# Performance work log

Hardware: AMD Instinct MI355X
Metric: run time of the kernel (lower is better)

## Reference

```python
import jax, jax.numpy as jnp
import numpy as np

NUM_STAGES = 3
EPS = 1e-6


def _l2norm(x, axis):
    return x / (EPS + jnp.linalg.norm(x, axis=axis, keepdims=True))


def _l1norm(x, axis):
    return x / (EPS + jnp.sum(x, axis=axis, keepdims=True))


def setup_inputs() -> dict:
    key = jax.random.key(0)
    k1, k2 = jax.random.split(key)
    B, C, H, W, K = 16, 512, 64, 64, 64
    feats = jax.random.normal(k1, (B, C, H, W), dtype=jnp.float32)
    # bases buffer: N(0, sqrt(2/K)) then l2-normalized along channel dim (done in reference)
    bases = jax.random.normal(k2, (1, C, K), dtype=jnp.float32) * np.sqrt(2.0 / K)
    return {"feats": feats, "bases": bases}


def reference(feats, bases):
    B, C, H, W = feats.shape
    f = feats.reshape(B, C, H * W)              # [B, C, N]
    b = _l2norm(bases, axis=1)                  # match buffer init normalization
    b = jnp.broadcast_to(b, (B, C, b.shape[2])) # [B, C, K]
    attention = None
    for _ in range(NUM_STAGES):
        attention = jnp.einsum('bcn,bck->bnk', f, b)        # [B, N, K]
        attention = jax.nn.softmax(attention, axis=2)
        attention_normed = _l1norm(attention, axis=1)
        b = jnp.einsum('bcn,bnk->bck', f, attention_normed)  # [B, C, K]
        b = _l2norm(b, axis=1)
    # EM loop runs under torch.no_grad in the original
    b = jax.lax.stop_gradient(b)
    attention = jax.lax.stop_gradient(attention)
    feats_recon = jnp.einsum('bck,bnk->bcn', b, attention)   # [B, C, N]
    return feats_recon.reshape(B, C, H, W)
```

## Files before the change

kernel.cpp:

```cpp
#include <hip/hip_runtime.h>
#include <stdint.h>

#define B_ 16
#define C_ 512
#define N_ 4096
#define K_ 64
#define NUM_STAGES 3

typedef __bf16 bf16x8 __attribute__((ext_vector_type(8)));
typedef float f32x4 __attribute__((ext_vector_type(4)));

__device__ __forceinline__ uint16_t f2bf(float x) {
  union { float f; uint32_t u; } v; v.f = x;
  uint32_t r = (v.u + 0x7FFFu + ((v.u >> 16) & 1u)) >> 16;
  return (uint16_t)r;
}

__device__ __forceinline__ void async16(const uint16_t* g, uint16_t* l) {
  __builtin_amdgcn_global_load_lds(
      (const __attribute__((address_space(1))) unsigned int*)g,
      (__attribute__((address_space(3))) unsigned int*)l, 16, 0, 0);
}

__global__ __launch_bounds__(256) void k_prep(const float* __restrict__ feats,
                                              uint16_t* __restrict__ f16,
                                              uint16_t* __restrict__ fT16) {
  __shared__ uint16_t tile[64][65];
  int b = blockIdx.z, c0 = blockIdx.y * 64, n0 = blockIdx.x * 64;
  int t = threadIdx.x;
  const float* src = feats + ((size_t)b * C_ + c0) * N_ + n0;
  uint16_t* dst = f16 + ((size_t)b * C_ + c0) * N_ + n0;
  int cl = t >> 4;
  int nl = (t & 15) * 4;
#pragma unroll
  for (int i = 0; i < 4; ++i) {
    int c = cl + 16 * i;
    float4 v = *(const float4*)(src + (size_t)c * N_ + nl);
    ushort4 x;
    x.x = f2bf(v.x); x.y = f2bf(v.y); x.z = f2bf(v.z); x.w = f2bf(v.w);
    *(ushort4*)(dst + (size_t)c * N_ + nl) = x;
    tile[c][nl + 0] = x.x; tile[c][nl + 1] = x.y;
    tile[c][nl + 2] = x.z; tile[c][nl + 3] = x.w;
  }
  __syncthreads();
  uint16_t* dstT = fT16 + ((size_t)b * N_ + n0) * C_ + c0;
#pragma unroll
  for (int i = 0; i < 4; ++i) {
    int n = cl + 16 * i;
    int c = nl;
    ushort4 y;
    y.x = tile[c + 0][n]; y.y = tile[c + 1][n];
    y.z = tile[c + 2][n]; y.w = tile[c + 3][n];
    *(ushort4*)(dstT + (size_t)n * C_ + c) = y;
  }
}

__global__ __launch_bounds__(256) void k_init_basis(const float* __restrict__ bases,
                                                    uint16_t* __restrict__ basis,
                                                    uint16_t* __restrict__ basisT) {
  int b = blockIdx.x;
  int t = threadIdx.x;
  __shared__ float red[256];
  __shared__ float inv[64];
  int k = t & 63;
  float s = 0.f;
  for (int c = (t >> 6); c < C_; c += 4) {
    float v = bases[c * K_ + k];
    s += v * v;
  }
  red[t] = s;
  __syncthreads();
  if (t < 64) {
    float tot = red[t] + red[t + 64] + red[t + 128] + red[t + 192];
    inv[t] = 1.f / (1e-6f + sqrtf(tot));
  }
  __syncthreads();
  uint16_t* ob = basis + (size_t)b * C_ * K_;
  for (int i = 0; i < (C_ * K_) / 256; ++i) {
    int idx = t + 256 * i;
    int kk = idx & 63;
    ob[idx] = f2bf(bases[idx] * inv[kk]);
  }
  uint16_t* obT = basisT + (size_t)b * K_ * C_;
  for (int i = 0; i < (C_ * K_) / 256; ++i) {
    int idx = t + 256 * i;
    int kk = idx >> 9;
    int cc = idx & 511;
    obT[idx] = f2bf(bases[cc * K_ + kk] * inv[kk]);
  }
}

__global__ __launch_bounds__(256) void k_gemm1(const uint16_t* __restrict__ fT,
                                               const uint16_t* __restrict__ basisT,
                                               uint16_t* __restrict__ attn,
                                               uint16_t* __restrict__ attnT) {
  __shared__ __attribute__((aligned(16))) uint16_t ldsA[64 * 64];
  __shared__ __attribute__((aligned(16))) uint16_t ldsB[64 * 64];
  int b = blockIdx.y;
  int n0 = blockIdx.x * 64;
  int t = threadIdx.x;
  int w = t >> 6, lane = t & 63, l15 = lane & 15, quad = lane >> 4;
  const uint16_t* A = fT + ((size_t)b * N_ + n0) * C_;
  const uint16_t* Bm = basisT + (size_t)b * K_ * C_;
  f32x4 acc[4] = {};
  for (int cs = 0; cs < C_; cs += 64) {
    __syncthreads();
#pragma unroll
    for (int r = 0; r < 2; ++r) {
      int e = r * 256 + t;
      int row = e >> 3, ch = e & 7;
      int sch = (ch + row) & 7;
      async16(A + (size_t)row * C_ + cs + sch * 8, ldsA + (r * 256 + (t & 192)) * 8);
    }
#pragma unroll
    for (int r = 0; r < 2; ++r) {
      int e = r * 256 + t;
      int row = e >> 3, ch = e & 7;
      int sch = (ch + row) & 7;
      async16(Bm + (size_t)row * C_ + cs + sch * 8, ldsB + (r * 256 + (t & 192)) * 8);
    }
    __syncthreads();
#pragma unroll
    for (int s = 0; s < 2; ++s) {
      int cc = s * 4 + quad;
      int ra = 16 * w + l15;
      bf16x8 af = *(const bf16x8*)(ldsA + ra * 64 + ((cc - ra) & 7) * 8);
#pragma unroll
      for (int t4 = 0; t4 < 4; ++t4) {
        int rb = 16 * t4 + l15;
        bf16x8 bv = *(const bf16x8*)(ldsB + rb * 64 + ((cc - rb) & 7) * 8);
        acc[t4] = __builtin_amdgcn_mfma_f32_16x16x32_bf16(af, bv, acc[t4], 0, 0, 0);
      }
    }
  }
  float p[4][4];
#pragma unroll
  for (int r = 0; r < 4; ++r) {
    float m = fmaxf(fmaxf(acc[0][r], acc[1][r]), fmaxf(acc[2][r], acc[3][r]));
    m = fmaxf(m, __shfl_xor(m, 1));
    m = fmaxf(m, __shfl_xor(m, 2));
    m = fmaxf(m, __shfl_xor(m, 4));
    m = fmaxf(m, __shfl_xor(m, 8));
    float s = 0.f;
#pragma unroll
    for (int t4 = 0; t4 < 4; ++t4) { p[t4][r] = __expf(acc[t4][r] - m); s += p[t4][r]; }
    s += __shfl_xor(s, 1); s += __shfl_xor(s, 2);
    s += __shfl_xor(s, 4); s += __shfl_xor(s, 8);
    float inv = 1.f / s;
#pragma unroll
    for (int t4 = 0; t4 < 4; ++t4) p[t4][r] *= inv;
  }
  uint16_t* oa = attn + ((size_t)b * N_ + n0 + 16 * w + quad * 4) * K_;
#pragma unroll
  for (int r = 0; r < 4; ++r) {
#pragma unroll
    for (int t4 = 0; t4 < 4; ++t4) oa[(size_t)r * K_ + 16 * t4 + l15] = f2bf(p[t4][r]);
  }
#pragma unroll
  for (int t4 = 0; t4 < 4; ++t4) {
    ushort4 y;
    y.x = f2bf(p[t4][0]); y.y = f2bf(p[t4][1]);
    y.z = f2bf(p[t4][2]); y.w = f2bf(p[t4][3]);
    *(ushort4*)(attnT + ((size_t)b * K_ + 16 * t4 + l15) * N_ + n0 + 16 * w + quad * 4) = y;
  }
}

__global__ __launch_bounds__(256) void k_gemm2(const uint16_t* __restrict__ f16,
                                               const uint16_t* __restrict__ attnT,
                                               float* __restrict__ brawT) {
  __shared__ __attribute__((aligned(16))) uint16_t ldsA[32 * 64];
  __shared__ __attribute__((aligned(16))) uint16_t ldsB[64 * 64];
  int b = blockIdx.z;
  int c0 = blockIdx.x * 32;
  int slice = blockIdx.y;
  int ns0 = slice * 1024;
  int t = threadIdx.x, w = t >> 6, lane = t & 63, l15 = lane & 15, quad = lane >> 4;
  int h = w >> 1, kh = w & 1;
  const uint16_t* A = f16 + ((size_t)b * C_ + c0) * N_;
  const uint16_t* Bm = attnT + (size_t)b * K_ * N_;
  f32x4 acc[2] = {};
  for (int ns = ns0; ns < ns0 + 1024; ns += 64) {
    __syncthreads();
    {
      int row = t >> 3, ch = t & 7;
      int sch = (ch + row) & 7;
      async16(A + (size_t)row * N_ + ns + sch * 8, ldsA + (t & 192) * 8);
    }
#pragma unroll
    for (int r = 0; r < 2; ++r) {
      int e = r * 256 + t;
      int row = e >> 3, ch = e & 7;
      int sch = (ch + row) & 7;
      async16(Bm + (size_t)row * N_ + ns + sch * 8, ldsB + (r * 256 + (t & 192)) * 8);
    }
    __syncthreads();
#pragma unroll
    for (int s = 0; s < 2; ++s) {
      int cc = s * 4 + quad;
      int ra = 16 * h + l15;
      bf16x8 af = *(const bf16x8*)(ldsA + ra * 64 + ((cc - ra) & 7) * 8);
#pragma unroll
      for (int t2 = 0; t2 < 2; ++t2) {
        int rb = 32 * kh + 16 * t2 + l15;
        bf16x8 bv = *(const bf16x8*)(ldsB + rb * 64 + ((cc - rb) & 7) * 8);
        acc[t2] = __builtin_amdgcn_mfma_f32_16x16x32_bf16(af, bv, acc[t2], 0, 0, 0);
      }
    }
  }
  float* out = brawT + ((size_t)slice * B_ + b) * K_ * C_;
#pragma unroll
  for (int t2 = 0; t2 < 2; ++t2) {
    int k = 32 * kh + 16 * t2 + l15;
    float4 v = make_float4(acc[t2][0], acc[t2][1], acc[t2][2], acc[t2][3]);
    *(float4*)(out + (size_t)k * C_ + c0 + 16 * h + quad * 4) = v;
  }
}

__global__ __launch_bounds__(256) void k_l2norm(const float* __restrict__ brawT,
                                                uint16_t* __restrict__ basisT) {
  int b = blockIdx.x;
  int t = threadIdx.x, w = t >> 6, lane = t & 63;
  for (int k = w; k < K_; k += 4) {
    float v[8];
#pragma unroll
    for (int j = 0; j < 8; ++j) v[j] = 0.f;
#pragma unroll
    for (int s = 0; s < 4; ++s) {
      const float* rs = brawT + (((size_t)s * B_ + b) * K_ + k) * C_ + lane * 8;
      float4 a = *(const float4*)(rs);
      float4 c4 = *(const float4*)(rs + 4);
      v[0] += a.x; v[1] += a.y; v[2] += a.z; v[3] += a.w;
      v[4] += c4.x; v[5] += c4.y; v[6] += c4.z; v[7] += c4.w;
    }
    float ss = 0.f;
#pragma unroll
    for (int j = 0; j < 8; ++j) ss += v[j] * v[j];
    ss += __shfl_xor(ss, 1); ss += __shfl_xor(ss, 2); ss += __shfl_xor(ss, 4);
    ss += __shfl_xor(ss, 8); ss += __shfl_xor(ss, 16); ss += __shfl_xor(ss, 32);
    float inv = 1.f / (1e-6f + sqrtf(ss));
    ushort4 y0, y1;
    y0.x = f2bf(v[0] * inv); y0.y = f2bf(v[1] * inv);
    y0.z = f2bf(v[2] * inv); y0.w = f2bf(v[3] * inv);
    y1.x = f2bf(v[4] * inv); y1.y = f2bf(v[5] * inv);
    y1.z = f2bf(v[6] * inv); y1.w = f2bf(v[7] * inv);
    uint16_t* o = basisT + ((size_t)b * K_ + k) * C_ + lane * 8;
    *(ushort4*)(o) = y0;
    *(ushort4*)(o + 4) = y1;
  }
}

__global__ __launch_bounds__(256) void k_transpose_basis(const uint16_t* __restrict__ basisT,
                                                         uint16_t* __restrict__ basis) {
  __shared__ uint16_t tile[64][65];
  int b = blockIdx.y, ct = blockIdx.x;
  int t = threadIdx.x;
  const uint16_t* src = basisT + (size_t)b * K_ * C_ + ct * 64;
  for (int i = 0; i < 16; ++i) {
    int idx = t + 256 * i;
    int k = idx >> 6, c = idx & 63;
    tile[k][c] = src[(size_t)k * C_ + c];
  }
  __syncthreads();
  uint16_t* dst = basis + (size_t)b * C_ * K_ + (size_t)ct * 64 * K_;
  for (int i = 0; i < 16; ++i) {
    int idx = t + 256 * i;
    int c = idx >> 6, k = idx & 63;
    dst[(size_t)c * K_ + k] = tile[k][c];
  }
}

__global__ __launch_bounds__(256) void k_recon(const uint16_t* __restrict__ attn,
                                               const uint16_t* __restrict__ basis,
                                               float* __restrict__ out) {
  __shared__ __attribute__((aligned(16))) uint16_t ldsA[64 * 64];
  __shared__ __attribute__((aligned(16))) uint16_t ldsB[64 * 64];
  int b = blockIdx.z, c0 = blockIdx.y * 64, n0 = blockIdx.x * 64;
  int t = threadIdx.x, w = t >> 6, lane = t & 63, l15 = lane & 15, quad = lane >> 4;
  const uint16_t* A = attn + ((size_t)b * N_ + n0) * K_;
  const uint16_t* Bm = basis + ((size_t)b * C_ + c0) * K_;
#pragma unroll
  for (int r = 0; r < 2; ++r) {
    int e = r * 256 + t;
    int row = e >> 3, ch = e & 7, sch = (ch + row) & 7;
    async16(A + (size_t)row * K_ + sch * 8, ldsA + (r * 256 + (t & 192)) * 8);
  }
#pragma unroll
  for (int r = 0; r < 2; ++r) {
    int e = r * 256 + t;
    int row = e >> 3, ch = e & 7, sch = (ch + row) & 7;
    async16(Bm + (size_t)row * K_ + sch * 8, ldsB + (r * 256 + (t & 192)) * 8);
  }
  f32x4 acc[4] = {};
  __syncthreads();
#pragma unroll
  for (int s = 0; s < 2; ++s) {
    int cc = s * 4 + quad;
    int ra = 16 * w + l15;
    bf16x8 af = *(const bf16x8*)(ldsA + ra * 64 + ((cc - ra) & 7) * 8);
#pragma unroll
    for (int t4 = 0; t4 < 4; ++t4) {
      int rb = 16 * t4 + l15;
      bf16x8 bv = *(const bf16x8*)(ldsB + rb * 64 + ((cc - rb) & 7) * 8);
      acc[t4] = __builtin_amdgcn_mfma_f32_16x16x32_bf16(af, bv, acc[t4], 0, 0, 0);
    }
  }
#pragma unroll
  for (int t4 = 0; t4 < 4; ++t4) {
    int c = c0 + 16 * t4 + l15;
    float4 v = make_float4(acc[t4][0], acc[t4][1], acc[t4][2], acc[t4][3]);
    *(float4*)(out + ((size_t)b * C_ + c) * N_ + n0 + 16 * w + quad * 4) = v;
  }
}

extern "C" void kernel_launch(void* const* d_in, const int* in_sizes, int n_in,
                              void* d_out, int out_size, void* d_ws, size_t ws_size,
                              hipStream_t stream) {
  const float* feats = (const float*)d_in[0];
  const float* bases = (const float*)d_in[1];
  float* out = (float*)d_out;
  char* ws = (char*)d_ws;
  uint16_t* f16 = (uint16_t*)(ws);
  uint16_t* fT16 = (uint16_t*)(ws + 67108864);
  uint16_t* attn = (uint16_t*)(ws + 134217728);
  uint16_t* attnT = (uint16_t*)(ws + 142606336);
  uint16_t* basis = (uint16_t*)(ws + 150994944);
  uint16_t* basisT = (uint16_t*)(ws + 152043520);
  float* brawT = (float*)(ws + 153092096);

  k_prep<<<dim3(64, 8, 16), 256, 0, stream>>>(feats, f16, fT16);
  k_init_basis<<<16, 256, 0, stream>>>(bases, basis, basisT);
  for (int st = 0; st < NUM_STAGES; ++st) {
    k_gemm1<<<dim3(64, 16), 256, 0, stream>>>(fT16, basisT, attn, attnT);
    k_gemm2<<<dim3(16, 4, 16), 256, 0, stream>>>(f16, attnT, brawT);
    k_l2norm<<<16, 256, 0, stream>>>(brawT, basisT);
    k_transpose_basis<<<dim3(8, 16), 256, 0, stream>>>(basisT, basis);
  }
  k_recon<<<dim3(64, 8, 16), 256, 0, stream>>>(attn, basis, out);
}
```

Measured before the change: 478.6 us.

## Enlarge GEMM tiles to 512 threads, skip redundant attn writes, batch prep tiles

gemm1 and recon now use 128-row N tiles with 512 threads, so each basis tile loaded into LDS serves twice as many rows. gemm2 is restructured to 128 channels by 64 K per block with 8 N-slices, so the f16 tile is reused across all K, and l2norm now sums 8 partial slices. gemm1 writes the row-major attention only on the last stage, dropping redundant stores in earlier stages. k_prep processes four 64-wide tiles per block with vectorized LDS writes. The trade-offs are fewer blocks per launch and gemm2 partial-sum stores that are now scalar and strided.

After: 507.4 us. 6.0% more time.

```diff
diff --git a/kernel.cpp b/kernel.cpp
--- a/kernel.cpp
+++ b/kernel.cpp
@@ -25,33 +25,36 @@
 __global__ __launch_bounds__(256) void k_prep(const float* __restrict__ feats,
                                               uint16_t* __restrict__ f16,
                                               uint16_t* __restrict__ fT16) {
-  __shared__ uint16_t tile[64][65];
-  int b = blockIdx.z, c0 = blockIdx.y * 64, n0 = blockIdx.x * 64;
-  int t = threadIdx.x;
-  const float* src = feats + ((size_t)b * C_ + c0) * N_ + n0;
-  uint16_t* dst = f16 + ((size_t)b * C_ + c0) * N_ + n0;
+  __shared__ uint16_t tile[64][68];
+  int b = blockIdx.z, c0 = blockIdx.y * 64, n0 = blockIdx.x * 256;
+  int t = threadIdx.x;
   int cl = t >> 4;
   int nl = (t & 15) * 4;
-#pragma unroll
-  for (int i = 0; i < 4; ++i) {
-    int c = cl + 16 * i;
-    float4 v = *(const float4*)(src + (size_t)c * N_ + nl);
-    ushort4 x;
-    x.x = f2bf(v.x); x.y = f2bf(v.y); x.z = f2bf(v.z); x.w = f2bf(v.w);
-    *(ushort4*)(dst + (size_t)c * N_ + nl) = x;
-    tile[c][nl + 0] = x.x; tile[c][nl + 1] = x.y;
-    tile[c][nl + 2] = x.z; tile[c][nl + 3] = x.w;
-  }
-  __syncthreads();
-  uint16_t* dstT = fT16 + ((size_t)b * N_ + n0) * C_ + c0;
-#pragma unroll
-  for (int i = 0; i < 4; ++i) {
-    int n = cl + 16 * i;
-    int c = nl;
-    ushort4 y;
-    y.x = tile[c + 0][n]; y.y = tile[c + 1][n];
-    y.z = tile[c + 2][n]; y.w = tile[c + 3][n];
-    *(ushort4*)(dstT + (size_t)n * C_ + c) = y;
+  for (int nt = 0; nt < 4; ++nt) {
+    int n0s = n0 + nt * 64;
+    const float* src = feats + ((size_t)b * C_ + c0) * N_ + n0s;
+    uint16_t* dst = f16 + ((size_t)b * C_ + c0) * N_ + n0s;
+    __syncthreads();
+#pragma unroll
+    for (int i = 0; i < 4; ++i) {
+      int c = cl + 16 * i;
+      float4 v = *(const float4*)(src + (size_t)c * N_ + nl);
+      ushort4 x;
+      x.x = f2bf(v.x); x.y = f2bf(v.y); x.z = f2bf(v.z); x.w = f2bf(v.w);
+      *(ushort4*)(dst + (size_t)c * N_ + nl) = x;
+      *(ushort4*)&tile[c][nl] = x;
+    }
+    __syncthreads();
+    uint16_t* dstT = fT16 + ((size_t)b * N_ + n0s) * C_ + c0;
+#pragma unroll
+    for (int i = 0; i < 4; ++i) {
+      int n = cl + 16 * i;
+      int c = nl;
+      ushort4 y;
+      y.x = tile[c + 0][n]; y.y = tile[c + 1][n];
+      y.z = tile[c + 2][n]; y.w = tile[c + 3][n];
+      *(ushort4*)(dstT + (size_t)n * C_ + c) = y;
+    }
   }
 }
 
@@ -90,14 +93,15 @@
   }
 }
 
-__global__ __launch_bounds__(256) void k_gemm1(const uint16_t* __restrict__ fT,
+__global__ __launch_bounds__(512) void k_gemm1(const uint16_t* __restrict__ fT,
                                                const uint16_t* __restrict__ basisT,
                                                uint16_t* __restrict__ attn,
-                                               uint16_t* __restrict__ attnT) {
-  __shared__ __attribute__((aligned(16))) uint16_t ldsA[64 * 64];
+                                               uint16_t* __restrict__ attnT,
+                                               int write_attn) {
+  __shared__ __attribute__((aligned(16))) uint16_t ldsA[128 * 64];
   __shared__ __attribute__((aligned(16))) uint16_t ldsB[64 * 64];
   int b = blockIdx.y;
-  int n0 = blockIdx.x * 64;
+  int n0 = blockIdx.x * 128;
   int t = threadIdx.x;
   int w = t >> 6, lane = t & 63, l15 = lane & 15, quad = lane >> 4;
   const uint16_t* A = fT + ((size_t)b * N_ + n0) * C_;
@@ -107,17 +111,15 @@
     __syncthreads();
 #pragma unroll
     for (int r = 0; r < 2; ++r) {
-      int e = r * 256 + t;
+      int e = r * 512 + t;
       int row = e >> 3, ch = e & 7;
       int sch = (ch + row) & 7;
-      async16(A + (size_t)row * C_ + cs + sch * 8, ldsA + (r * 256 + (t & 192)) * 8);
-    }
-#pragma unroll
-    for (int r = 0; r < 2; ++r) {
-      int e = r * 256 + t;
-      int row = e >> 3, ch = e & 7;
+      async16(A + (size_t)row * C_ + cs + sch * 8, ldsA + (r * 512 + (t & 448)) * 8);
+    }
+    {
+      int row = t >> 3, ch = t & 7;
       int sch = (ch + row) & 7;
-      async16(Bm + (size_t)row * C_ + cs + sch * 8, ldsB + (r * 256 + (t & 192)) * 8);
+      async16(Bm + (size_t)row * C_ + cs + sch * 8, ldsB + (t & 448) * 8);
     }
     __syncthreads();
 #pragma unroll
@@ -150,11 +152,13 @@
 #pragma unroll
     for (int t4 = 0; t4 < 4; ++t4) p[t4][r] *= inv;
   }
-  uint16_t* oa = attn + ((size_t)b * N_ + n0 + 16 * w + quad * 4) * K_;
-#pragma unroll
-  for (int r = 0; r < 4; ++r) {
-#pragma unroll
-    for (int t4 = 0; t4 < 4; ++t4) oa[(size_t)r * K_ + 16 * t4 + l15] = f2bf(p[t4][r]);
+  if (write_attn) {
+    uint16_t* oa = attn + ((size_t)b * N_ + n0 + 16 * w + quad * 4) * K_;
+#pragma unroll
+    for (int r = 0; r < 4; ++r) {
+#pragma unroll
+      for (int t4 = 0; t4 < 4; ++t4) oa[(size_t)r * K_ + 16 * t4 + l15] = f2bf(p[t4][r]);
+    }
   }
 #pragma unroll
   for (int t4 = 0; t4 < 4; ++t4) {
@@ -165,54 +169,55 @@
   }
 }
 
-__global__ __launch_bounds__(256) void k_gemm2(const uint16_t* __restrict__ f16,
+__global__ __launch_bounds__(512) void k_gemm2(const uint16_t* __restrict__ f16,
                                                const uint16_t* __restrict__ attnT,
                                                float* __restrict__ brawT) {
-  __shared__ __attribute__((aligned(16))) uint16_t ldsA[32 * 64];
-  __shared__ __attribute__((aligned(16))) uint16_t ldsB[64 * 64];
+  __shared__ __attribute__((aligned(16))) uint16_t ldsF[128 * 64];
+  __shared__ __attribute__((aligned(16))) uint16_t ldsP[64 * 64];
   int b = blockIdx.z;
-  int c0 = blockIdx.x * 32;
   int slice = blockIdx.y;
-  int ns0 = slice * 1024;
-  int t = threadIdx.x, w = t >> 6, lane = t & 63, l15 = lane & 15, quad = lane >> 4;
-  int h = w >> 1, kh = w & 1;
-  const uint16_t* A = f16 + ((size_t)b * C_ + c0) * N_;
-  const uint16_t* Bm = attnT + (size_t)b * K_ * N_;
-  f32x4 acc[2] = {};
-  for (int ns = ns0; ns < ns0 + 1024; ns += 64) {
-    __syncthreads();
+  int c0 = blockIdx.x * 128;
+  int t = threadIdx.x;
+  int w = t >> 6, lane = t & 63, l15 = lane & 15, quad = lane >> 4;
+  const uint16_t* F = f16 + ((size_t)b * C_ + c0) * N_;
+  const uint16_t* P = attnT + (size_t)b * K_ * N_;
+  f32x4 acc[4] = {};
+  int ns0 = slice * 512;
+  for (int ns = ns0; ns < ns0 + 512; ns += 64) {
+    __syncthreads();
+#pragma unroll
+    for (int r = 0; r < 2; ++r) {
+      int e = r * 512 + t;
+      int row = e >> 3, ch = e & 7;
+      int sch = (ch + row) & 7;
+      async16(F + (size_t)row * N_ + ns + sch * 8, ldsF + (r * 512 + (t & 448)) * 8);
+    }
     {
       int row = t >> 3, ch = t & 7;
       int sch = (ch + row) & 7;
-      async16(A + (size_t)row * N_ + ns + sch * 8, ldsA + (t & 192) * 8);
-    }
-#pragma unroll
-    for (int r = 0; r < 2; ++r) {
-      int e = r * 256 + t;
-      int row = e >> 3, ch = e & 7;
-      int sch = (ch + row) & 7;
-      async16(Bm + (size_t)row * N_ + ns + sch * 8, ldsB + (r * 256 + (t & 192)) * 8);
+      async16(P + (size_t)row * N_ + ns + sch * 8, ldsP + (t & 448) * 8);
     }
     __syncthreads();
 #pragma unroll
     for (int s = 0; s < 2; ++s) {
       int cc = s * 4 + quad;
-      int ra = 16 * h + l15;
-      bf16x8 af = *(const bf16x8*)(ldsA + ra * 64 + ((cc - ra) & 7) * 8);
-#pragma unroll
-      for (int t2 = 0; t2 < 2; ++t2) {
-        int rb = 32 * kh + 16 * t2 + l15;
-        bf16x8 bv = *(const bf16x8*)(ldsB + rb * 64 + ((cc - rb) & 7) * 8);
-        acc[t2] = __builtin_amdgcn_mfma_f32_16x16x32_bf16(af, bv, acc[t2], 0, 0, 0);
+      int rb = 16 * w + l15;
+      bf16x8 fv = *(const bf16x8*)(ldsF + rb * 64 + ((cc - rb) & 7) * 8);
+#pragma unroll
+      for (int kt = 0; kt < 4; ++kt) {
+        int ra = 16 * kt + l15;
+        bf16x8 av = *(const bf16x8*)(ldsP + ra * 64 + ((cc - ra) & 7) * 8);
+        acc[kt] = __builtin_amdgcn_mfma_f32_16x16x32_bf16(av, fv, acc[kt], 0, 0, 0);
       }
     }
   }
-  float* out = brawT + ((size_t)slice * B_ + b) * K_ * C_;
-#pragma unroll
-  for (int t2 = 0; t2 < 2; ++t2) {
-    int k = 32 * kh + 16 * t2 + l15;
-    float4 v = make_float4(acc[t2][0], acc[t2][1], acc[t2][2], acc[t2][3]);
-    *(float4*)(out + (size_t)k * C_ + c0 + 16 * h + quad * 4) = v;
+  float* outp = brawT + ((size_t)slice * B_ + b) * K_ * C_;
+#pragma unroll
+  for (int kt = 0; kt < 4; ++kt) {
+#pragma unroll
+    for (int r = 0; r < 4; ++r) {
+      outp[(size_t)(16 * kt + quad * 4 + r) * C_ + c0 + 16 * w + l15] = acc[kt][r];
+    }
   }
 }
 
@@ -225,7 +230,7 @@
 #pragma unroll
     for (int j = 0; j < 8; ++j) v[j] = 0.f;
 #pragma unroll
-    for (int s = 0; s < 4; ++s) {
+    for (int s = 0; s < 8; ++s) {
       const float* rs = brawT + (((size_t)s * B_ + b) * K_ + k) * C_ + lane * 8;
       float4 a = *(const float4*)(rs);
       float4 c4 = *(const float4*)(rs + 4);
@@ -269,26 +274,24 @@
   }
 }
 
-__global__ __launch_bounds__(256) void k_recon(const uint16_t* __restrict__ attn,
+__global__ __launch_bounds__(512) void k_recon(const uint16_t* __restrict__ attn,
                                                const uint16_t* __restrict__ basis,
                                                float* __restrict__ out) {
-  __shared__ __attribute__((aligned(16))) uint16_t ldsA[64 * 64];
+  __shared__ __attribute__((aligned(16))) uint16_t ldsA[128 * 64];
   __shared__ __attribute__((aligned(16))) uint16_t ldsB[64 * 64];
-  int b = blockIdx.z, c0 = blockIdx.y * 64, n0 = blockIdx.x * 64;
+  int b = blockIdx.z, c0 = blockIdx.y * 64, n0 = blockIdx.x * 128;
   int t = threadIdx.x, w = t >> 6, lane = t & 63, l15 = lane & 15, quad = lane >> 4;
   const uint16_t* A = attn + ((size_t)b * N_ + n0) * K_;
   const uint16_t* Bm = basis + ((size_t)b * C_ + c0) * K_;
 #pragma unroll
   for (int r = 0; r < 2; ++r) {
-    int e = r * 256 + t;
+    int e = r * 512 + t;
     int row = e >> 3, ch = e & 7, sch = (ch + row) & 7;
-    async16(A + (size_t)row * K_ + sch * 8, ldsA + (r * 256 + (t & 192)) * 8);
-  }
-#pragma unroll
-  for (int r = 0; r < 2; ++r) {
-    int e = r * 256 + t;
-    int row = e >> 3, ch = e & 7, sch = (ch + row) & 7;
-    async16(Bm + (size_t)row * K_ + sch * 8, ldsB + (r * 256 + (t & 192)) * 8);
+    async16(A + (size_t)row * K_ + sch * 8, ldsA + (r * 512 + (t & 448)) * 8);
+  }
+  {
+    int row = t >> 3, ch = t & 7, sch = (ch + row) & 7;
+    async16(Bm + (size_t)row * K_ + sch * 8, ldsB + (t & 448) * 8);
   }
   f32x4 acc[4] = {};
   __syncthreads();
@@ -327,13 +330,14 @@
   uint16_t* basisT = (uint16_t*)(ws + 152043520);
   float* brawT = (float*)(ws + 153092096);
 
-  k_prep<<<dim3(64, 8, 16), 256, 0, stream>>>(feats, f16, fT16);
+  k_prep<<<dim3(16, 8, 16), 256, 0, stream>>>(feats, f16, fT16);
   k_init_basis<<<16, 256, 0, stream>>>(bases, basis, basisT);
   for (int st = 0; st < NUM_STAGES; ++st) {
-    k_gemm1<<<dim3(64, 16), 256, 0, stream>>>(fT16, basisT, attn, attnT);
-    k_gemm2<<<dim3(16, 4, 16), 256, 0, stream>>>(f16, attnT, brawT);
+    k_gemm1<<<dim3(32, 16), 512, 0, stream>>>(fT16, basisT, attn, attnT,
+                                              st == NUM_STAGES - 1 ? 1 : 0);
+    k_gemm2<<<dim3(4, 8, 16), 512, 0, stream>>>(f16, attnT, brawT);
     k_l2norm<<<16, 256, 0, stream>>>(brawT, basisT);
     k_transpose_basis<<<dim3(8, 16), 256, 0, stream>>>(basisT, basis);
   }
-  k_recon<<<dim3(64, 8, 16), 256, 0, stream>>>(attn, basis, out);
-}
+  k_recon<<<dim3(32, 8, 16), 512, 0, stream>>>(attn, basis, out);
+}
```

## Fuse l2norm with basis transpose, skip unused attn writes, stage recon output

Applied to the files above, without the earlier changes.

Merges the l2norm and basis-transpose kernels into one kernel with a wider grid (16x16 blocks) that writes both basis layouts. The row-major attention is now written only in the last stage, since recon is its only consumer. The recon kernel stages its output tile in LDS so that global stores are coalesced rows. The LDS index expressions are rewritten in an equivalent form. In exchange, the fused kernel writes the row-major basis with strided scalar stores and adds an extra LDS round-trip in recon.

Result: faster. 448.4 us (-6.3%).

```diff
diff --git a/kernel.cpp b/kernel.cpp
--- a/kernel.cpp
+++ b/kernel.cpp
@@ -93,7 +93,8 @@
 __global__ __launch_bounds__(256) void k_gemm1(const uint16_t* __restrict__ fT,
                                                const uint16_t* __restrict__ basisT,
                                                uint16_t* __restrict__ attn,
-                                               uint16_t* __restrict__ attnT) {
+                                               uint16_t* __restrict__ attnT,
+                                               int write_attn) {
   __shared__ __attribute__((aligned(16))) uint16_t ldsA[64 * 64];
   __shared__ __attribute__((aligned(16))) uint16_t ldsB[64 * 64];
   int b = blockIdx.y;
@@ -124,11 +125,11 @@
     for (int s = 0; s < 2; ++s) {
       int cc = s * 4 + quad;
       int ra = 16 * w + l15;
-      bf16x8 af = *(const bf16x8*)(ldsA + ra * 64 + ((cc - ra) & 7) * 8);
+      bf16x8 af = *(const bf16x8*)(ldsA + (ra * 8 + ((cc - ra) & 7)) * 8);
 #pragma unroll
       for (int t4 = 0; t4 < 4; ++t4) {
         int rb = 16 * t4 + l15;
-        bf16x8 bv = *(const bf16x8*)(ldsB + rb * 64 + ((cc - rb) & 7) * 8);
+        bf16x8 bv = *(const bf16x8*)(ldsB + (rb * 8 + ((cc - rb) & 7)) * 8);
         acc[t4] = __builtin_amdgcn_mfma_f32_16x16x32_bf16(af, bv, acc[t4], 0, 0, 0);
       }
     }
@@ -150,11 +151,13 @@
 #pragma unroll
     for (int t4 = 0; t4 < 4; ++t4) p[t4][r] *= inv;
   }
-  uint16_t* oa = attn + ((size_t)b * N_ + n0 + 16 * w + quad * 4) * K_;
-#pragma unroll
-  for (int r = 0; r < 4; ++r) {
-#pragma unroll
-    for (int t4 = 0; t4 < 4; ++t4) oa[(size_t)r * K_ + 16 * t4 + l15] = f2bf(p[t4][r]);
+  if (write_attn) {
+    uint16_t* oa = attn + ((size_t)b * N_ + n0 + 16 * w + quad * 4) * K_;
+#pragma unroll
+    for (int r = 0; r < 4; ++r) {
+#pragma unroll
+      for (int t4 = 0; t4 < 4; ++t4) oa[(size_t)r * K_ + 16 * t4 + l15] = f2bf(p[t4][r]);
+    }
   }
 #pragma unroll
   for (int t4 = 0; t4 < 4; ++t4) {
@@ -198,11 +201,11 @@
     for (int s = 0; s < 2; ++s) {
       int cc = s * 4 + quad;
       int ra = 16 * h + l15;
-      bf16x8 af = *(const bf16x8*)(ldsA + ra * 64 + ((cc - ra) & 7) * 8);
+      bf16x8 af = *(const bf16x8*)(ldsA + (ra * 8 + ((cc - ra) & 7)) * 8);
 #pragma unroll
       for (int t2 = 0; t2 < 2; ++t2) {
         int rb = 32 * kh + 16 * t2 + l15;
-        bf16x8 bv = *(const bf16x8*)(ldsB + rb * 64 + ((cc - rb) & 7) * 8);
+        bf16x8 bv = *(const bf16x8*)(ldsB + (rb * 8 + ((cc - rb) & 7)) * 8);
         acc[t2] = __builtin_amdgcn_mfma_f32_16x16x32_bf16(af, bv, acc[t2], 0, 0, 0);
       }
     }
@@ -216,64 +219,64 @@
   }
 }
 
-__global__ __launch_bounds__(256) void k_l2norm(const float* __restrict__ brawT,
-                                                uint16_t* __restrict__ basisT) {
-  int b = blockIdx.x;
-  int t = threadIdx.x, w = t >> 6, lane = t & 63;
-  for (int k = w; k < K_; k += 4) {
-    float v[8];
-#pragma unroll
-    for (int j = 0; j < 8; ++j) v[j] = 0.f;
+__global__ __launch_bounds__(256) void k_l2fused(const float* __restrict__ brawT,
+                                                 uint16_t* __restrict__ basisT,
+                                                 uint16_t* __restrict__ basis) {
+  __shared__ float red[4][128];
+  __shared__ float invs[4];
+  int b = blockIdx.x, kg = blockIdx.y;
+  int t = threadIdx.x;
+  int c4 = (t & 127) * 4;
+  int khalf = t >> 7;
+  float4 bs[2];
+  float pr[2];
+#pragma unroll
+  for (int i = 0; i < 2; ++i) {
+    int k = kg * 4 + khalf * 2 + i;
+    float4 a = make_float4(0.f, 0.f, 0.f, 0.f);
 #pragma unroll
     for (int s = 0; s < 4; ++s) {
-      const float* rs = brawT + (((size_t)s * B_ + b) * K_ + k) * C_ + lane * 8;
-      float4 a = *(const float4*)(rs);
-      float4 c4 = *(const float4*)(rs + 4);
-      v[0] += a.x; v[1] += a.y; v[2] += a.z; v[3] += a.w;
-      v[4] += c4.x; v[5] += c4.y; v[6] += c4.z; v[7] += c4.w;
-    }
-    float ss = 0.f;
-#pragma unroll
-    for (int j = 0; j < 8; ++j) ss += v[j] * v[j];
-    ss += __shfl_xor(ss, 1); ss += __shfl_xor(ss, 2); ss += __shfl_xor(ss, 4);
-    ss += __shfl_xor(ss, 8); ss += __shfl_xor(ss, 16); ss += __shfl_xor(ss, 32);
-    float inv = 1.f / (1e-6f + sqrtf(ss));
-    ushort4 y0, y1;
-    y0.x = f2bf(v[0] * inv); y0.y = f2bf(v[1] * inv);
-    y0.z = f2bf(v[2] * inv); y0.w = f2bf(v[3] * inv);
-    y1.x = f2bf(v[4] * inv); y1.y = f2bf(v[5] * inv);
-    y1.z = f2bf(v[6] * inv); y1.w = f2bf(v[7] * inv);
-    uint16_t* o = basisT + ((size_t)b * K_ + k) * C_ + lane * 8;
-    *(ushort4*)(o) = y0;
-    *(ushort4*)(o + 4) = y1;
-  }
-}
-
-__global__ __launch_bounds__(256) void k_transpose_basis(const uint16_t* __restrict__ basisT,
-                                                         uint16_t* __restrict__ basis) {
-  __shared__ uint16_t tile[64][65];
-  int b = blockIdx.y, ct = blockIdx.x;
-  int t = threadIdx.x;
-  const uint16_t* src = basisT + (size_t)b * K_ * C_ + ct * 64;
-  for (int i = 0; i < 16; ++i) {
-    int idx = t + 256 * i;
-    int k = idx >> 6, c = idx & 63;
-    tile[k][c] = src[(size_t)k * C_ + c];
-  }
-  __syncthreads();
-  uint16_t* dst = basis + (size_t)b * C_ * K_ + (size_t)ct * 64 * K_;
-  for (int i = 0; i < 16; ++i) {
-    int idx = t + 256 * i;
-    int c = idx >> 6, k = idx & 63;
-    dst[(size_t)c * K_ + k] = tile[k][c];
+      const float* rp = brawT + (((size_t)s * B_ + b) * K_ + k) * C_ + c4;
+      float4 v = *(const float4*)rp;
+      a.x += v.x; a.y += v.y; a.z += v.z; a.w += v.w;
+    }
+    bs[i] = a;
+    pr[i] = a.x * a.x + a.y * a.y + a.z * a.z + a.w * a.w;
+  }
+  red[khalf * 2 + 0][t & 127] = pr[0];
+  red[khalf * 2 + 1][t & 127] = pr[1];
+  __syncthreads();
+  if (t < 4) {
+    float s = 0.f;
+#pragma unroll
+    for (int j = 0; j < 128; ++j) s += red[t][j];
+    invs[t] = 1.f / (1e-6f + sqrtf(s));
+  }
+  __syncthreads();
+#pragma unroll
+  for (int i = 0; i < 2; ++i) {
+    int kk = khalf * 2 + i;
+    int k = kg * 4 + kk;
+    float inv = invs[kk];
+    ushort4 y;
+    y.x = f2bf(bs[i].x * inv); y.y = f2bf(bs[i].y * inv);
+    y.z = f2bf(bs[i].z * inv); y.w = f2bf(bs[i].w * inv);
+    *(ushort4*)(basisT + ((size_t)b * K_ + k) * C_ + c4) = y;
+    uint16_t* ob = basis + (size_t)b * C_ * K_ + k;
+    ob[(size_t)(c4 + 0) * K_] = y.x;
+    ob[(size_t)(c4 + 1) * K_] = y.y;
+    ob[(size_t)(c4 + 2) * K_] = y.z;
+    ob[(size_t)(c4 + 3) * K_] = y.w;
   }
 }
 
 __global__ __launch_bounds__(256) void k_recon(const uint16_t* __restrict__ attn,
                                                const uint16_t* __restrict__ basis,
                                                float* __restrict__ out) {
-  __shared__ __attribute__((aligned(16))) uint16_t ldsA[64 * 64];
-  __shared__ __attribute__((aligned(16))) uint16_t ldsB[64 * 64];
+  __shared__ __attribute__((aligned(16))) char smem[64 * 68 * 4];
+  uint16_t* ldsA = (uint16_t*)smem;
+  uint16_t* ldsB = (uint16_t*)(smem + 8192);
+  float* ldsT = (float*)smem;
   int b = blockIdx.z, c0 = blockIdx.y * 64, n0 = blockIdx.x * 64;
   int t = threadIdx.x, w = t >> 6, lane = t & 63, l15 = lane & 15, quad = lane >> 4;
   const uint16_t* A = attn + ((size_t)b * N_ + n0) * K_;
@@ -296,19 +299,26 @@
   for (int s = 0; s < 2; ++s) {
     int cc = s * 4 + quad;
     int ra = 16 * w + l15;
-    bf16x8 af = *(const bf16x8*)(ldsA + ra * 64 + ((cc - ra) & 7) * 8);
+    bf16x8 af = *(const bf16x8*)(ldsA + (ra * 8 + ((cc - ra) & 7)) * 8);
 #pragma unroll
     for (int t4 = 0; t4 < 4; ++t4) {
       int rb = 16 * t4 + l15;
-      bf16x8 bv = *(const bf16x8*)(ldsB + rb * 64 + ((cc - rb) & 7) * 8);
+      bf16x8 bv = *(const bf16x8*)(ldsB + (rb * 8 + ((cc - rb) & 7)) * 8);
       acc[t4] = __builtin_amdgcn_mfma_f32_16x16x32_bf16(af, bv, acc[t4], 0, 0, 0);
     }
   }
+  __syncthreads();
 #pragma unroll
   for (int t4 = 0; t4 < 4; ++t4) {
-    int c = c0 + 16 * t4 + l15;
     float4 v = make_float4(acc[t4][0], acc[t4][1], acc[t4][2], acc[t4][3]);
-    *(float4*)(out + ((size_t)b * C_ + c) * N_ + n0 + 16 * w + quad * 4) = v;
+    *(float4*)(ldsT + (size_t)(16 * t4 + l15) * 68 + 16 * w + quad * 4) = v;
+  }
+  __syncthreads();
+  float* op = out + ((size_t)b * C_ + c0) * N_ + n0;
+#pragma unroll
+  for (int j = 0; j < 16; ++j) {
+    int c = 4 * j + w;
+    op[(size_t)c * N_ + lane] = ldsT[(size_t)c * 68 + lane];
   }
 }
 
@@ -330,10 +340,10 @@
   k_prep<<<dim3(64, 8, 16), 256, 0, stream>>>(feats, f16, fT16);
   k_init_basis<<<16, 256, 0, stream>>>(bases, basis, basisT);
   for (int st = 0; st < NUM_STAGES; ++st) {
-    k_gemm1<<<dim3(64, 16), 256, 0, stream>>>(fT16, basisT, attn, attnT);
+    k_gemm1<<<dim3(64, 16), 256, 0, stream>>>(fT16, basisT, attn, attnT,
+                                              st == NUM_STAGES - 1 ? 1 : 0);
     k_gemm2<<<dim3(16, 4, 16), 256, 0, stream>>>(f16, attnT, brawT);
-    k_l2norm<<<16, 256, 0, stream>>>(brawT, basisT);
-    k_transpose_basis<<<dim3(8, 16), 256, 0, stream>>>(basisT, basis);
+    k_l2fused<<<dim3(16, 16), 256, 0, stream>>>(brawT, basisT, basis);
   }
   k_recon<<<dim3(64, 8, 16), 256, 0, stream>>>(attn, basis, out);
 }
```
